# Kernel optimization log

Hardware: AMD Instinct MI355X
Metric: run time of the kernel (lower is better)

Reference implementation:

```python
import jax, jax.numpy as jnp
import numpy as np
import math

B, T, D, H = 2, 2048, 1024, 16
DH = D // H  # 64


def _rope_tables(seq_len, dim, dtype=jnp.float32):
    inv_freq = 1.0 / (10000.0 ** (jnp.arange(0, dim, 2, dtype=jnp.float32) / dim))
    t = jnp.arange(seq_len, dtype=jnp.float32)
    freqs = jnp.outer(t, inv_freq)  # [T, dim/2]
    return jnp.cos(freqs).astype(dtype), jnp.sin(freqs).astype(dtype)


def apply_rotary(x, cos, sin):
    # x: [B,H,T,DH]; cos/sin: [1,1,T,DH/2]
    d = x.shape[-1]
    x1, x2 = x[..., : d // 2], x[..., d // 2 :]
    return jnp.concatenate([x1 * cos - x2 * sin, x2 * cos + x1 * sin], axis=-1)


def setup_inputs() -> dict:
    key = jax.random.key(0)
    k1, k2, k3 = jax.random.split(key, 3)
    x = jax.random.normal(k1, (B, T, D), dtype=jnp.float32)
    Wqkv = jax.random.normal(k2, (D, 3 * D), dtype=jnp.float32) * (1.0 / math.sqrt(D))
    Wout = jax.random.normal(k3, (D, D), dtype=jnp.float32) * (1.0 / math.sqrt(D))
    cos, sin = _rope_tables(T, DH)  # [T, 32]
    mask = jnp.tril(jnp.ones((T, T), dtype=bool))[None, None]  # causal [1,1,T,T]
    return {"x": x, "Wqkv": Wqkv, "Wout": Wout, "cos": cos, "sin": sin, "mask": mask}


def reference(x, Wqkv, Wout, cos, sin, mask):
    Bb, Tt, C = x.shape
    qkv = (x @ Wqkv).reshape(Bb, Tt, 3, H, DH)
    q = jnp.transpose(qkv[:, :, 0], (0, 2, 1, 3))  # [B,H,T,DH]
    k = jnp.transpose(qkv[:, :, 1], (0, 2, 1, 3))
    v = jnp.transpose(qkv[:, :, 2], (0, 2, 1, 3))
    c = cos[None, None]  # [1,1,T,DH/2]
    s = sin[None, None]
    q = apply_rotary(q, c, s)
    k = apply_rotary(k, c, s)
    attn = jnp.einsum("bhqd,bhkd->bhqk", q, k) / math.sqrt(DH)
    attn = jnp.where(mask, attn, jnp.float32(-jnp.inf))
    attn = jax.nn.softmax(attn, axis=-1)  # dropout p=0 (eval)
    out = jnp.einsum("bhqk,bhkd->bhqd", attn, v)
    out = jnp.transpose(out, (0, 2, 1, 3)).reshape(Bb, Tt, C)
    return out @ Wout
```

## Files before the change

### kernel.cpp

```cpp
#include <hip/hip_runtime.h>
#include <hip/hip_bf16.h>

#define B_ 2
#define T_ 2048
#define D_ 1024
#define H_ 16
#define DH_ 64
#define N3_ 3072
#define M_ 4096

typedef __attribute__((ext_vector_type(8))) short short8;
typedef __attribute__((ext_vector_type(4))) float f32x4;
typedef __attribute__((ext_vector_type(4))) unsigned short ushort4v;

__device__ __forceinline__ unsigned short f2bf(float f) {
  return __builtin_bit_cast(unsigned short, __hip_bfloat16(f));
}
__device__ __forceinline__ float bf2f(unsigned short u) {
  union { unsigned u; float f; } v; v.u = ((unsigned)u) << 16;
  return v.f;
}

__device__ __forceinline__ void gload_lds16(const unsigned short* g, unsigned short* l) {
  __builtin_amdgcn_global_load_lds((const __attribute__((address_space(1))) void*)g,
                                   (__attribute__((address_space(3))) void*)l, 16, 0, 0);
}

__global__ __launch_bounds__(256)
void k_cvt(const float* __restrict__ in, unsigned short* __restrict__ out) {
  int i = (blockIdx.x * 256 + threadIdx.x) * 4;
  f32x4 v = *(const f32x4*)&in[i];
  ushort4v o;
  o[0] = f2bf(v[0]); o[1] = f2bf(v[1]); o[2] = f2bf(v[2]); o[3] = f2bf(v[3]);
  *(ushort4v*)&out[i] = o;
}

__global__ __launch_bounds__(256)
void k_transpose(const float* __restrict__ in, unsigned short* __restrict__ out,
                 int R, int C) {
  __shared__ float tile[64][65];
  int c0 = blockIdx.x * 64, r0 = blockIdx.y * 64;
  int tx = threadIdx.x & 63, ty = threadIdx.x >> 6;
#pragma unroll
  for (int i = 0; i < 64; i += 4)
    tile[ty + i][tx] = in[(size_t)(r0 + ty + i) * C + c0 + tx];
  __syncthreads();
#pragma unroll
  for (int i = 0; i < 64; i += 4)
    out[(size_t)(c0 + ty + i) * R + r0 + tx] = f2bf(tile[tx][ty + i]);
}

template <typename OUT_T>
__global__ __launch_bounds__(256)
void k_gemm_bt(const unsigned short* __restrict__ A, const unsigned short* __restrict__ Bt,
               OUT_T* __restrict__ C, int Mx, int Nx, int Kx) {
  __shared__ __align__(16) unsigned short As[128 * 64];
  __shared__ __align__(16) unsigned short Bs[128 * 64];
  const int tid = threadIdx.x;
  const int lane = tid & 63;
  const int l15 = lane & 15, lg = lane >> 4;
  const int l8 = lane >> 3, c8 = lane & 7;
  const int wid = tid >> 6;
  const int wr = wid >> 1, wc = wid & 1;
  const int m0 = blockIdx.y * 128, n0 = blockIdx.x * 128;

  const f32x4 zero4 = {0.f, 0.f, 0.f, 0.f};
  f32x4 acc[4][4];
#pragma unroll
  for (int mi = 0; mi < 4; ++mi)
#pragma unroll
    for (int ni = 0; ni < 4; ++ni) acc[mi][ni] = zero4;

  for (int k0 = 0; k0 < Kx; k0 += 64) {
#pragma unroll
    for (int i = 0; i < 4; ++i)
      gload_lds16(&A[(size_t)(m0 + wid * 32 + i * 8 + l8) * Kx + k0 + c8 * 8],
                  &As[(wid * 32 + i * 8) * 64]);
#pragma unroll
    for (int i = 0; i < 4; ++i)
      gload_lds16(&Bt[(size_t)(n0 + wid * 32 + i * 8 + l8) * Kx + k0 + c8 * 8],
                  &Bs[(wid * 32 + i * 8) * 64]);
    __syncthreads();
#pragma unroll
    for (int kk = 0; kk < 2; ++kk) {
      short8 af[4], bfr[4];
#pragma unroll
      for (int mi = 0; mi < 4; ++mi)
        af[mi] = *(const short8*)&As[(wr * 64 + mi * 16 + l15) * 64 + kk * 32 + lg * 8];
#pragma unroll
      for (int ni = 0; ni < 4; ++ni)
        bfr[ni] = *(const short8*)&Bs[(wc * 64 + ni * 16 + l15) * 64 + kk * 32 + lg * 8];
#pragma unroll
      for (int mi = 0; mi < 4; ++mi)
#pragma unroll
        for (int ni = 0; ni < 4; ++ni)
          acc[mi][ni] = __builtin_amdgcn_mfma_f32_16x16x32_bf16(af[mi], bfr[ni], acc[mi][ni], 0, 0, 0);
    }
    __syncthreads();
  }
#pragma unroll
  for (int mi = 0; mi < 4; ++mi)
#pragma unroll
    for (int ni = 0; ni < 4; ++ni)
#pragma unroll
      for (int j = 0; j < 4; ++j) {
        int row = m0 + wr * 64 + mi * 16 + lg * 4 + j;
        int col = n0 + wc * 64 + ni * 16 + l15;
        float v = acc[mi][ni][j];
        if constexpr (sizeof(OUT_T) == 2) C[(size_t)row * Nx + col] = f2bf(v);
        else                              C[(size_t)row * Nx + col] = v;
      }
}

__global__ __launch_bounds__(256)
void k_gemm_qkv_rope(const unsigned short* __restrict__ A, const unsigned short* __restrict__ Bt,
                     const float* __restrict__ cosT, const float* __restrict__ sinT,
                     unsigned short* __restrict__ Q, unsigned short* __restrict__ K,
                     unsigned short* __restrict__ Vt) {
  __shared__ __align__(16) unsigned short As[128 * 64];
  __shared__ __align__(16) unsigned short Bs[128 * 64];
  const int Kx = D_, Nx = N3_;
  const int tid = threadIdx.x;
  const int lane = tid & 63;
  const int l15 = lane & 15, lg = lane >> 4;
  const int l8 = lane >> 3, c8 = lane & 7;
  const int wid = tid >> 6;
  const int wr = wid >> 1, wc = wid & 1;
  const int m0 = blockIdx.y * 128, n0 = blockIdx.x * 128;

  const f32x4 zero4 = {0.f, 0.f, 0.f, 0.f};
  f32x4 acc[4][4];
#pragma unroll
  for (int mi = 0; mi < 4; ++mi)
#pragma unroll
    for (int ni = 0; ni < 4; ++ni) acc[mi][ni] = zero4;

  for (int k0 = 0; k0 < Kx; k0 += 64) {
#pragma unroll
    for (int i = 0; i < 4; ++i)
      gload_lds16(&A[(size_t)(m0 + wid * 32 + i * 8 + l8) * Kx + k0 + c8 * 8],
                  &As[(wid * 32 + i * 8) * 64]);
#pragma unroll
    for (int i = 0; i < 4; ++i)
      gload_lds16(&Bt[(size_t)(n0 + wid * 32 + i * 8 + l8) * Kx + k0 + c8 * 8],
                  &Bs[(wid * 32 + i * 8) * 64]);
    __syncthreads();
#pragma unroll
    for (int kk = 0; kk < 2; ++kk) {
      short8 af[4], bfr[4];
#pragma unroll
      for (int mi = 0; mi < 4; ++mi)
        af[mi] = *(const short8*)&As[(wr * 64 + mi * 16 + l15) * 64 + kk * 32 + lg * 8];
#pragma unroll
      for (int ni = 0; ni < 4; ++ni)
        bfr[ni] = *(const short8*)&Bs[(wc * 64 + ni * 16 + l15) * 64 + kk * 32 + lg * 8];
#pragma unroll
      for (int mi = 0; mi < 4; ++mi)
#pragma unroll
        for (int ni = 0; ni < 4; ++ni)
          acc[mi][ni] = __builtin_amdgcn_mfma_f32_16x16x32_bf16(af[mi], bfr[ni], acc[mi][ni], 0, 0, 0);
    }
    __syncthreads();
  }

  const int region = n0 >> 10;
  const int h = (((n0 & 1023)) + wc * 64) >> 6;
  if (region < 2) {
    unsigned short* out = (region == 0) ? Q : K;
    const float scale = (region == 0) ? 0.125f : 1.f;
#pragma unroll
    for (int mi = 0; mi < 4; ++mi)
#pragma unroll
      for (int j = 0; j < 4; ++j) {
        int row = m0 + wr * 64 + mi * 16 + lg * 4 + j;
        int b = row >> 11, t = row & (T_ - 1);
        size_t obase = ((size_t)(b * H_ + h) * T_ + t) * DH_;
#pragma unroll
        for (int ni = 0; ni < 2; ++ni) {
          int dh = ni * 16 + l15;
          float cs = cosT[t * 32 + dh], sn = sinT[t * 32 + dh];
          float x1 = acc[mi][ni][j], x2 = acc[mi][ni + 2][j];
          out[obase + dh]      = f2bf((x1 * cs - x2 * sn) * scale);
          out[obase + dh + 32] = f2bf((x2 * cs + x1 * sn) * scale);
        }
      }
  } else {
#pragma unroll
    for (int mi = 0; mi < 4; ++mi) {
      int row0 = m0 + wr * 64 + mi * 16 + lg * 4;
      int b = row0 >> 11, t0 = row0 & (T_ - 1);
#pragma unroll
      for (int ni = 0; ni < 4; ++ni) {
        int col = (n0 - 2048) + wc * 64 + ni * 16 + l15;
        int hv = col >> 6, dh = col & 63;
        ushort4v pk;
#pragma unroll
        for (int j = 0; j < 4; ++j) pk[j] = f2bf(acc[mi][ni][j]);
        *(ushort4v*)&Vt[((size_t)(b * H_ + hv) * DH_ + dh) * T_ + t0] = pk;
      }
    }
  }
}

__global__ __launch_bounds__(256)
void k_attn(const unsigned short* __restrict__ Q, const unsigned short* __restrict__ K,
            const unsigned short* __restrict__ Vt, unsigned short* __restrict__ O) {
  __shared__ __align__(16) unsigned short Ks[2 * 64 * 64];
  __shared__ __align__(16) unsigned short Vs[2 * 64 * 64];
  __shared__ __align__(16) unsigned short Pl[4][16][72];
  const int tid = threadIdx.x;
  const int wid = tid >> 6, lane = tid & 63;
  const int l15 = lane & 15, lg = lane >> 4;
  const int l8 = lane >> 3, c8 = lane & 7;
  const int srcoff = (c8 ^ l8) << 3;
  const int wg = (blockIdx.x & 7) * 128 + (blockIdx.x >> 3);
  const int qb = 31 - (wg & 31);
  const int hb = wg >> 5;
  const int qblk = qb * 64;
  const int q0 = qblk + wid * 16;
  const size_t hbase = (size_t)hb * T_ * DH_;
  const unsigned short* Qh = Q + hbase;
  const unsigned short* Kh = K + hbase;
  const unsigned short* Vh = Vt + hbase;
  unsigned short* Pw = &Pl[wid][0][0];

  short8 bq0 = *(const short8*)&Qh[(q0 + l15) * DH_ + lg * 8];
  short8 bq1 = *(const short8*)&Qh[(q0 + l15) * DH_ + 32 + lg * 8];

  int koffA[4], koffB[4], voff[2][4];
#pragma unroll
  for (int g = 0; g < 4; ++g) {
    int r = g * 16 + l15;
    koffA[g] = r * 64 + (((lg)     ^ (r & 7)) << 3);
    koffB[g] = r * 64 + (((4 + lg) ^ (r & 7)) << 3);
  }
#pragma unroll
  for (int ks = 0; ks < 2; ++ks)
#pragma unroll
    for (int nb = 0; nb < 4; ++nb) {
      int r = nb * 16 + l15;
      voff[ks][nb] = r * 64 + (((ks * 4 + lg) ^ (r & 7)) << 3);
    }

  const f32x4 zero4 = {0.f, 0.f, 0.f, 0.f};
  f32x4 accO[4];
#pragma unroll
  for (int nb = 0; nb < 4; ++nb) accO[nb] = zero4;
  float m_run = -INFINITY, l_run = 0.f;
  const int qg = q0 + l15;
  const int kend_w = q0 + 16;
  const int kend_blk = qblk + 64;

  auto stage = [&](int buf, int kt) {
    if (wid < 2) {
      const unsigned short* Kt = Kh + (size_t)kt * DH_;
#pragma unroll
      for (int i = 0; i < 4; ++i)
        gload_lds16(&Kt[(wid * 32 + i * 8 + l8) * DH_ + srcoff],
                    &Ks[buf * 4096 + (wid * 4 + i) * 512]);
    } else {
      const unsigned short* Vg = Vh + kt;
#pragma unroll
      for (int i = 0; i < 4; ++i)
        gload_lds16(&Vg[((wid - 2) * 32 + i * 8 + l8) * T_ + srcoff],
                    &Vs[buf * 4096 + ((wid - 2) * 4 + i) * 512]);
    }
  };

  stage(0, 0);
  for (int kt = 0; kt < kend_blk; kt += 64) {
    const int cur = (kt >> 6) & 1;
    __syncthreads();
    if (kt + 64 < kend_blk) stage(cur ^ 1, kt + 64);
    if (kt >= kend_w) continue;
    const unsigned short* Kb_ = &Ks[cur * 4096];
    const unsigned short* Vb_ = &Vs[cur * 4096];

    f32x4 cg[4];
#pragma unroll
    for (int g = 0; g < 4; ++g) {
      short8 a0 = *(const short8*)&Kb_[koffA[g]];
      short8 a1 = *(const short8*)&Kb_[koffB[g]];
      cg[g] = __builtin_amdgcn_mfma_f32_16x16x32_bf16(a0, bq0, zero4, 0, 0, 0);
      cg[g] = __builtin_amdgcn_mfma_f32_16x16x32_bf16(a1, bq1, cg[g], 0, 0, 0);
    }
    float s[16];
#pragma unroll
    for (int g = 0; g < 4; ++g)
#pragma unroll
      for (int j = 0; j < 4; ++j) s[g * 4 + j] = cg[g][j];
    if (kt + 63 > q0) {
#pragma unroll
      for (int g = 0; g < 4; ++g) {
        int kb0 = kt + g * 16 + lg * 4;
#pragma unroll
        for (int j = 0; j < 4; ++j)
          if (kb0 + j > qg) s[g * 4 + j] = -INFINITY;
      }
    }
    float t8[8];
#pragma unroll
    for (int j = 0; j < 8; ++j) t8[j] = fmaxf(s[j], s[j + 8]);
    float t4a = fmaxf(t8[0], t8[4]), t4b = fmaxf(t8[1], t8[5]);
    float t4c = fmaxf(t8[2], t8[6]), t4d = fmaxf(t8[3], t8[7]);
    float pm = fmaxf(fmaxf(t4a, t4b), fmaxf(t4c, t4d));
    pm = fmaxf(pm, __shfl_xor(pm, 16));
    pm = fmaxf(pm, __shfl_xor(pm, 32));
    if (!__all(pm <= m_run + 8.f)) {
      float m_new = fmaxf(m_run, pm);
      float alpha = __expf(m_run - m_new);
      float aj[4];
#pragma unroll
      for (int j = 0; j < 4; ++j) aj[j] = __shfl(alpha, lg * 4 + j);
#pragma unroll
      for (int nb = 0; nb < 4; ++nb)
#pragma unroll
        for (int j = 0; j < 4; ++j) accO[nb][j] *= aj[j];
      l_run *= alpha;
      m_run = m_new;
    }
    float p[16];
#pragma unroll
    for (int j = 0; j < 16; ++j) p[j] = __expf(s[j] - m_run);
    float u8[8];
#pragma unroll
    for (int j = 0; j < 8; ++j) u8[j] = p[j] + p[j + 8];
    float u4a = u8[0] + u8[4], u4b = u8[1] + u8[5];
    float u4c = u8[2] + u8[6], u4d = u8[3] + u8[7];
    float psum = (u4a + u4b) + (u4c + u4d);
    psum += __shfl_xor(psum, 16);
    psum += __shfl_xor(psum, 32);
    l_run += psum;

#pragma unroll
    for (int g = 0; g < 4; ++g) {
      ushort4v pk;
#pragma unroll
      for (int j = 0; j < 4; ++j) pk[j] = f2bf(p[g * 4 + j]);
      *(ushort4v*)&Pw[l15 * 72 + g * 16 + lg * 4] = pk;
    }
#pragma unroll
    for (int ks = 0; ks < 2; ++ks) {
      short8 pa = *(const short8*)&Pw[l15 * 72 + ks * 32 + lg * 8];
#pragma unroll
      for (int nb = 0; nb < 4; ++nb) {
        short8 vb = *(const short8*)&Vb_[voff[ks][nb]];
        accO[nb] = __builtin_amdgcn_mfma_f32_16x16x32_bf16(pa, vb, accO[nb], 0, 0, 0);
      }
    }
  }
  float lj[4];
#pragma unroll
  for (int j = 0; j < 4; ++j) lj[j] = 1.f / __shfl(l_run, lg * 4 + j);
  int b = hb >> 4, h = hb & 15;
#pragma unroll
  for (int nb = 0; nb < 4; ++nb)
#pragma unroll
    for (int j = 0; j < 4; ++j) {
      int t = q0 + lg * 4 + j;
      O[(size_t)(b * T_ + t) * D_ + h * DH_ + nb * 16 + l15] = f2bf(accO[nb][j] * lj[j]);
    }
}

extern "C" void kernel_launch(void* const* d_in, const int* in_sizes, int n_in,
                              void* d_out, int out_size, void* d_ws, size_t ws_size,
                              hipStream_t stream) {
  const float* x    = (const float*)d_in[0];
  const float* Wqkv = (const float*)d_in[1];
  const float* Wout = (const float*)d_in[2];
  const float* cosT = (const float*)d_in[3];
  const float* sinT = (const float*)d_in[4];
  float* out = (float*)d_out;
  char* ws = (char*)d_ws;
  unsigned short* Xb     = (unsigned short*)(ws);
  unsigned short* Wqkv_t = (unsigned short*)(ws + 8388608);
  unsigned short* Wout_t = (unsigned short*)(ws + 14680064);
  unsigned short* Ob     = (unsigned short*)(ws + 16777216);
  unsigned short* Qb     = (unsigned short*)(ws + 41943040);
  unsigned short* Kb     = (unsigned short*)(ws + 50331648);
  unsigned short* Vt     = (unsigned short*)(ws + 58720256);

  k_cvt<<<4096, 256, 0, stream>>>(x, Xb);
  k_transpose<<<dim3(48, 16), 256, 0, stream>>>(Wqkv, Wqkv_t, 1024, 3072);
  k_transpose<<<dim3(16, 16), 256, 0, stream>>>(Wout, Wout_t, 1024, 1024);
  k_gemm_qkv_rope<<<dim3(24, 32), 256, 0, stream>>>(Xb, Wqkv_t, cosT, sinT, Qb, Kb, Vt);
  k_attn<<<1024, 256, 0, stream>>>(Qb, Kb, Vt, Ob);
  k_gemm_bt<float><<<dim3(8, 32), 256, 0, stream>>>(Ob, Wout_t, out, 4096, 1024, 1024);
}
```

Before: 149.8 us.

## Load K/V directly from global memory in attention, drop LDS staging

Removes the double-buffered LDS staging of K and V tiles (global_load_lds plus a block barrier each iteration) and has each wave read its K rows and V columns straight from global memory into registers. Each wave now loops only up to its own causal end, with no block-wide synchronisation. The aim is to remove barrier stalls and LDS traffic, at the cost of four waves re-reading the same K/V data through cache with no prefetch overlap.

```diff
diff --git a/kernel.cpp b/kernel.cpp
--- a/kernel.cpp
+++ b/kernel.cpp
@@ -205,19 +205,14 @@
 __global__ __launch_bounds__(256)
 void k_attn(const unsigned short* __restrict__ Q, const unsigned short* __restrict__ K,
             const unsigned short* __restrict__ Vt, unsigned short* __restrict__ O) {
-  __shared__ __align__(16) unsigned short Ks[2 * 64 * 64];
-  __shared__ __align__(16) unsigned short Vs[2 * 64 * 64];
   __shared__ __align__(16) unsigned short Pl[4][16][72];
   const int tid = threadIdx.x;
   const int wid = tid >> 6, lane = tid & 63;
   const int l15 = lane & 15, lg = lane >> 4;
-  const int l8 = lane >> 3, c8 = lane & 7;
-  const int srcoff = (c8 ^ l8) << 3;
   const int wg = (blockIdx.x & 7) * 128 + (blockIdx.x >> 3);
   const int qb = 31 - (wg & 31);
   const int hb = wg >> 5;
-  const int qblk = qb * 64;
-  const int q0 = qblk + wid * 16;
+  const int q0 = qb * 64 + wid * 16;
   const size_t hbase = (size_t)hb * T_ * DH_;
   const unsigned short* Qh = Q + hbase;
   const unsigned short* Kh = K + hbase;
@@ -227,21 +222,6 @@
   short8 bq0 = *(const short8*)&Qh[(q0 + l15) * DH_ + lg * 8];
   short8 bq1 = *(const short8*)&Qh[(q0 + l15) * DH_ + 32 + lg * 8];
 
-  int koffA[4], koffB[4], voff[2][4];
-#pragma unroll
-  for (int g = 0; g < 4; ++g) {
-    int r = g * 16 + l15;
-    koffA[g] = r * 64 + (((lg)     ^ (r & 7)) << 3);
-    koffB[g] = r * 64 + (((4 + lg) ^ (r & 7)) << 3);
-  }
-#pragma unroll
-  for (int ks = 0; ks < 2; ++ks)
-#pragma unroll
-    for (int nb = 0; nb < 4; ++nb) {
-      int r = nb * 16 + l15;
-      voff[ks][nb] = r * 64 + (((ks * 4 + lg) ^ (r & 7)) << 3);
-    }
-
   const f32x4 zero4 = {0.f, 0.f, 0.f, 0.f};
   f32x4 accO[4];
 #pragma unroll
@@ -249,38 +229,14 @@
   float m_run = -INFINITY, l_run = 0.f;
   const int qg = q0 + l15;
   const int kend_w = q0 + 16;
-  const int kend_blk = qblk + 64;
-
-  auto stage = [&](int buf, int kt) {
-    if (wid < 2) {
-      const unsigned short* Kt = Kh + (size_t)kt * DH_;
-#pragma unroll
-      for (int i = 0; i < 4; ++i)
-        gload_lds16(&Kt[(wid * 32 + i * 8 + l8) * DH_ + srcoff],
-                    &Ks[buf * 4096 + (wid * 4 + i) * 512]);
-    } else {
-      const unsigned short* Vg = Vh + kt;
-#pragma unroll
-      for (int i = 0; i < 4; ++i)
-        gload_lds16(&Vg[((wid - 2) * 32 + i * 8 + l8) * T_ + srcoff],
-                    &Vs[buf * 4096 + ((wid - 2) * 4 + i) * 512]);
-    }
-  };
-
-  stage(0, 0);
-  for (int kt = 0; kt < kend_blk; kt += 64) {
-    const int cur = (kt >> 6) & 1;
-    __syncthreads();
-    if (kt + 64 < kend_blk) stage(cur ^ 1, kt + 64);
-    if (kt >= kend_w) continue;
-    const unsigned short* Kb_ = &Ks[cur * 4096];
-    const unsigned short* Vb_ = &Vs[cur * 4096];
-
+
+  for (int kt = 0; kt < kend_w; kt += 64) {
     f32x4 cg[4];
 #pragma unroll
     for (int g = 0; g < 4; ++g) {
-      short8 a0 = *(const short8*)&Kb_[koffA[g]];
-      short8 a1 = *(const short8*)&Kb_[koffB[g]];
+      const unsigned short* Kr = &Kh[(size_t)(kt + g * 16 + l15) * DH_];
+      short8 a0 = *(const short8*)&Kr[lg * 8];
+      short8 a1 = *(const short8*)&Kr[32 + lg * 8];
       cg[g] = __builtin_amdgcn_mfma_f32_16x16x32_bf16(a0, bq0, zero4, 0, 0, 0);
       cg[g] = __builtin_amdgcn_mfma_f32_16x16x32_bf16(a1, bq1, cg[g], 0, 0, 0);
     }
@@ -344,7 +300,7 @@
       short8 pa = *(const short8*)&Pw[l15 * 72 + ks * 32 + lg * 8];
 #pragma unroll
       for (int nb = 0; nb < 4; ++nb) {
-        short8 vb = *(const short8*)&Vb_[voff[ks][nb]];
+        short8 vb = *(const short8*)&Vh[(size_t)(nb * 16 + l15) * T_ + kt + ks * 32 + lg * 8];
         accO[nb] = __builtin_amdgcn_mfma_f32_16x16x32_bf16(pa, vb, accO[nb], 0, 0, 0);
       }
     }
```

Result: slower. 321.1 us (+114.4%).

## Software-pipeline attention loop to overlap next tile QK^T with softmax and PV

Applied to the files above, without the earlier changes.

Restructures the attention key loop into a two-stage software pipeline. The QK^T MFMAs for tile t+1 are issued while the softmax and PV of tile t are processed, and the loop is unrolled by two with two score register sets. The V tile buffer becomes triple-buffered so staging the next tile cannot overwrite V data still being consumed. The aim is to hide softmax latency (exp, reductions, LDS round-trip for P) behind matrix work. The cost is higher register and LDS use, which may reduce occupancy.

```diff
diff --git a/kernel.cpp b/kernel.cpp
--- a/kernel.cpp
+++ b/kernel.cpp
@@ -206,7 +206,7 @@
 void k_attn(const unsigned short* __restrict__ Q, const unsigned short* __restrict__ K,
             const unsigned short* __restrict__ Vt, unsigned short* __restrict__ O) {
   __shared__ __align__(16) unsigned short Ks[2 * 64 * 64];
-  __shared__ __align__(16) unsigned short Vs[2 * 64 * 64];
+  __shared__ __align__(16) unsigned short Vs[3 * 64 * 64];
   __shared__ __align__(16) unsigned short Pl[4][16][72];
   const int tid = threadIdx.x;
   const int wid = tid >> 6, lane = tid & 63;
@@ -248,35 +248,29 @@
   for (int nb = 0; nb < 4; ++nb) accO[nb] = zero4;
   float m_run = -INFINITY, l_run = 0.f;
   const int qg = q0 + l15;
-  const int kend_w = q0 + 16;
-  const int kend_blk = qblk + 64;
-
-  auto stage = [&](int buf, int kt) {
+  const int nt = qb + 1;
+
+  auto stage = [&](int t) {
+    const int kt = t << 6;
     if (wid < 2) {
+      unsigned short* kb = &Ks[(t & 1) * 4096];
       const unsigned short* Kt = Kh + (size_t)kt * DH_;
 #pragma unroll
       for (int i = 0; i < 4; ++i)
         gload_lds16(&Kt[(wid * 32 + i * 8 + l8) * DH_ + srcoff],
-                    &Ks[buf * 4096 + (wid * 4 + i) * 512]);
+                    &kb[(wid * 4 + i) * 512]);
     } else {
+      unsigned short* vb = &Vs[(t % 3) * 4096];
       const unsigned short* Vg = Vh + kt;
 #pragma unroll
       for (int i = 0; i < 4; ++i)
         gload_lds16(&Vg[((wid - 2) * 32 + i * 8 + l8) * T_ + srcoff],
-                    &Vs[buf * 4096 + ((wid - 2) * 4 + i) * 512]);
+                    &vb[((wid - 2) * 4 + i) * 512]);
     }
   };
 
-  stage(0, 0);
-  for (int kt = 0; kt < kend_blk; kt += 64) {
-    const int cur = (kt >> 6) & 1;
-    __syncthreads();
-    if (kt + 64 < kend_blk) stage(cur ^ 1, kt + 64);
-    if (kt >= kend_w) continue;
-    const unsigned short* Kb_ = &Ks[cur * 4096];
-    const unsigned short* Vb_ = &Vs[cur * 4096];
-
-    f32x4 cg[4];
+  auto QKT = [&](int t, f32x4* cg) {
+    const unsigned short* Kb_ = &Ks[(t & 1) * 4096];
 #pragma unroll
     for (int g = 0; g < 4; ++g) {
       short8 a0 = *(const short8*)&Kb_[koffA[g]];
@@ -284,6 +278,11 @@
       cg[g] = __builtin_amdgcn_mfma_f32_16x16x32_bf16(a0, bq0, zero4, 0, 0, 0);
       cg[g] = __builtin_amdgcn_mfma_f32_16x16x32_bf16(a1, bq1, cg[g], 0, 0, 0);
     }
+  };
+
+  auto SOFTPV = [&](int t, f32x4* cg) {
+    const int kt = t << 6;
+    const unsigned short* Vb_ = &Vs[(t % 3) * 4096];
     float s[16];
 #pragma unroll
     for (int g = 0; g < 4; ++g)
@@ -331,7 +330,6 @@
     psum += __shfl_xor(psum, 16);
     psum += __shfl_xor(psum, 32);
     l_run += psum;
-
 #pragma unroll
     for (int g = 0; g < 4; ++g) {
       ushort4v pk;
@@ -348,7 +346,22 @@
         accO[nb] = __builtin_amdgcn_mfma_f32_16x16x32_bf16(pa, vb, accO[nb], 0, 0, 0);
       }
     }
+  };
+
+  f32x4 cgA[4], cgB[4];
+  stage(0);
+  for (int t = 0; t < nt; t += 2) {
+    __syncthreads();
+    if (t + 1 < nt) stage(t + 1);
+    QKT(t, cgA);
+    if (t > 0) SOFTPV(t - 1, cgB);
+    __syncthreads();
+    if (t + 2 < nt) stage(t + 2);
+    if (t + 1 < nt) QKT(t + 1, cgB);
+    SOFTPV(t, cgA);
   }
+  if ((nt & 1) == 0) SOFTPV(nt - 1, cgB);
+
   float lj[4];
 #pragma unroll
   for (int j = 0; j < 4; ++j) lj[j] = 1.f / __shfl(l_run, lg * 4 + j);
```

Result: no change. 149.7 us (-0.1%).
